# Kernel optimization log

Hardware: AMD Instinct MI355X
Metric: run time of the kernel (lower is better)

## Reference

```python
import jax, jax.numpy as jnp
import numpy as np

NUM_LEVEL = 16
LOG_T = 19
TABLE_SIZE = 2 ** LOG_T
FEAT = 2
MIN_RES = 16
MAX_RES = 512
N_POINTS = 262144

# [Teschner et al. 2003] spatial hash primes, wrapped to int32 like torch does
HASH_COEFFS = jnp.asarray(np.array([1, 2654435761, 805459861], dtype=np.uint32).astype(np.int32))


def _resolutions():
    coeff = (MAX_RES / MIN_RES) ** (1.0 / (NUM_LEVEL - 1))
    return jnp.floor(MIN_RES * (jnp.float32(coeff) ** jnp.arange(NUM_LEVEL, dtype=jnp.float32)))


def _spatial_hash(verts_i32):
    # verts_i32: (..., 3) int32; wrap-around int32 multiply then xor, then mod T (non-negative)
    x = HASH_COEFFS * verts_i32
    idx = jnp.bitwise_xor(jnp.bitwise_xor(x[..., 0], x[..., 1]), x[..., 2])
    return jnp.mod(idx, TABLE_SIZE)


def _hash_encode(coords, tables):
    # coords: (N,3) f32 in [0,1); tables: (L,T,F) f16
    res = _resolutions()                                   # (L,)
    scaled = coords[None, :, :] * res[:, None, None]        # (L,N,3)
    floor = jnp.floor(scaled)
    ceil = jnp.ceil(scaled)
    # 8 voxel corners via floor/ceil selection bits
    offs = jnp.asarray(np.array([[(o >> 2) & 1, (o >> 1) & 1, o & 1] for o in range(8)], dtype=np.bool_))
    sel = offs[:, None, None, :]                            # (8,1,1,3)
    corner = jnp.where(sel, ceil[None], floor[None])        # (8,L,N,3)
    comp = jnp.where(sel, floor[None], ceil[None])          # opposite corner (8,L,N,3)
    idx = _spatial_hash(corner.astype(jnp.int32))           # (8,L,N)
    # gather per-level features: tables[l][idx[:,l,:]] -> (L,8,N,F)
    feats = jax.vmap(lambda tab, i: tab[i], in_axes=(0, 1))(tables, idx)
    # trilinear weight of corner o = prod |opposite_corner - scaled|
    w = jnp.prod(jnp.abs(comp - scaled[None]), axis=-1)     # (8,L,N)
    w = jnp.transpose(w, (1, 0, 2))                         # (L,8,N)
    lvl = jnp.sum(feats.astype(jnp.float32) * w[..., None], axis=1)  # (L,N,F)
    return jnp.transpose(lvl, (1, 0, 2)).reshape(coords.shape[0], NUM_LEVEL * FEAT)


def _mlp(x, w_in, b_in, w_h0, b_h0, w_h1, b_h1, w_out, b_out):
    h = jax.nn.relu(x @ w_in.T + b_in)
    h = jax.nn.relu(h @ w_h0.T + b_h0)
    h = jax.nn.relu(h @ w_h1.T + b_h1)
    return h @ w_out.T + b_out


def setup_inputs() -> dict:
    key = jax.random.key(0)
    ks = jax.random.split(key, 8)
    coords = jax.random.uniform(ks[0], (N_POINTS, 3), dtype=jnp.float32)
    tables = (2e-4 * jax.random.uniform(ks[1], (NUM_LEVEL, TABLE_SIZE, FEAT), dtype=jnp.float32) - 1e-4).astype(jnp.float16)
    def lin(k, out_d, in_d):
        return jax.random.normal(k, (out_d, in_d), dtype=jnp.float32) * (1.0 / np.sqrt(in_d))
    return {
        'coords': coords, 'tables': tables,
        'w_in': lin(ks[2], 64, 32), 'b_in': jnp.zeros((64,), jnp.float32),
        'w_h0': lin(ks[3], 64, 64), 'b_h0': jnp.zeros((64,), jnp.float32),
        'w_h1': lin(ks[4], 64, 64), 'b_h1': jnp.zeros((64,), jnp.float32),
        'w_out': lin(ks[5], 16, 64), 'b_out': jnp.zeros((16,), jnp.float32),
    }


def reference(coords, tables, w_in, b_in, w_h0, b_h0, w_h1, b_h1, w_out, b_out):
    enc = _hash_encode(coords, tables)  # (N, 32)
    return _mlp(enc, w_in, b_in, w_h0, b_h0, w_h1, b_h1, w_out, b_out)  # (N, 16)
```

## Files before the change

kernel.cpp:

```cpp
#include <hip/hip_runtime.h>

#define NLVL 16
#define LOGT 19
#define TMASK ((1u << LOGT) - 1u)
#define SCALE 4096.0f
#define INV_SCALE (1.0f / 4096.0f)
#define NFRAG 22

typedef _Float16 half_t;
typedef half_t half8 __attribute__((ext_vector_type(8)));
typedef half_t half4 __attribute__((ext_vector_type(4)));
typedef half_t half2v __attribute__((ext_vector_type(2)));
typedef float  float4v __attribute__((ext_vector_type(4)));

__device__ __constant__ float RES_C[NLVL] = {16.f, 20.f, 25.f, 32.f, 40.f, 50.f, 64.f, 80.f,
                                             101.f, 128.f, 161.f, 203.f, 256.f, 322.f, 406.f, 512.f};

__device__ __forceinline__ float4v mfma16(half8 a, half8 b, float4v c) {
    return __builtin_amdgcn_mfma_f32_16x16x32_f16(a, b, c, 0, 0, 0);
}

__global__ __launch_bounds__(64, 1) void nerf_wprep(
    const float* __restrict__ w_in, const float* __restrict__ w_h0,
    const float* __restrict__ w_h1, const float* __restrict__ w_out,
    half8* __restrict__ frags)
{
    const int frag = blockIdx.x;
    const int lane = threadIdx.x;
    const int m    = lane & 15;
    const int quad = lane >> 4;

    const float* W; int ncol, row, col;
    if (frag < 4)       { W = w_in;  ncol = 32; row = frag * 16 + m;            col = quad * 8; }
    else if (frag < 12) { const int f = frag - 4;
                          W = w_h0;  ncol = 64; row = (f >> 1) * 16 + m;        col = (f & 1) * 32 + quad * 8; }
    else if (frag < 20) { const int f = frag - 12;
                          W = w_h1;  ncol = 64; row = (f >> 1) * 16 + m;        col = (f & 1) * 32 + quad * 8; }
    else                { const int f = frag - 20;
                          W = w_out; ncol = 64; row = m;                        col = f * 32 + quad * 8; }

    const float* p = W + row * ncol + col;
    half8 r;
    #pragma unroll
    for (int j = 0; j < 8; ++j) r[j] = (half_t)p[j];
    frags[frag * 64 + lane] = r;
}

__global__ __launch_bounds__(256, 8) void nerf_encode_pair2(
    const float* __restrict__ coords,
    const float2* __restrict__ tab,
    half_t* __restrict__ encT, int npts)
{
    const int bpl  = npts >> 8;
    const int l    = blockIdx.x / bpl;
    const int side = threadIdx.x & 1;
    const int base = (blockIdx.x % bpl) * 256 + (threadIdx.x >> 1);
    const int p0 = base, p1 = base + 128;

    const float r = RES_C[l];
    const float2* __restrict__ bp = tab + (((unsigned)l) << LOGT);

    const float ax = coords[p0 * 3 + 0] * r, ay = coords[p0 * 3 + 1] * r, az = coords[p0 * 3 + 2] * r;
    const float afx = floorf(ax), afy = floorf(ay), afz = floorf(az);
    const float agx = ceilf(ax),  agy = ceilf(ay),  agz = ceilf(az);
    const unsigned ahx = side ? (unsigned)(int)agx : (unsigned)(int)afx;
    const float    awx = side ? (ax - afx) : (agx - ax);
    const unsigned ahfy = (unsigned)(int)afy * 2654435761u;
    const unsigned ahgy = (unsigned)(int)agy * 2654435761u;
    const unsigned ahfz = (unsigned)(int)afz * 805459861u;
    const unsigned ahgz = (unsigned)(int)agz * 805459861u;
    const float aty = ay - afy, atz = az - afz, auy = agy - ay, auz = agz - az;

    const float bx = coords[p1 * 3 + 0] * r, by = coords[p1 * 3 + 1] * r, bz = coords[p1 * 3 + 2] * r;
    const float bfx = floorf(bx), bfy = floorf(by), bfz = floorf(bz);
    const float bgx = ceilf(bx),  bgy = ceilf(by),  bgz = ceilf(bz);
    const unsigned bhx = side ? (unsigned)(int)bgx : (unsigned)(int)bfx;
    const float    bwx = side ? (bx - bfx) : (bgx - bx);
    const unsigned bhfy = (unsigned)(int)bfy * 2654435761u;
    const unsigned bhgy = (unsigned)(int)bgy * 2654435761u;
    const unsigned bhfz = (unsigned)(int)bfz * 805459861u;
    const unsigned bhgz = (unsigned)(int)bgz * 805459861u;
    const float bty = by - bfy, btz = bz - bfz, buy = bgy - by, buz = bgz - bz;

    const float2 a0 = bp[(ahx ^ ahfy ^ ahfz) & TMASK];
    const float2 a1 = bp[(ahx ^ ahfy ^ ahgz) & TMASK];
    const float2 a2 = bp[(ahx ^ ahgy ^ ahfz) & TMASK];
    const float2 a3 = bp[(ahx ^ ahgy ^ ahgz) & TMASK];
    const float2 b0 = bp[(bhx ^ bhfy ^ bhfz) & TMASK];
    const float2 b1 = bp[(bhx ^ bhfy ^ bhgz) & TMASK];
    const float2 b2 = bp[(bhx ^ bhgy ^ bhfz) & TMASK];
    const float2 b3 = bp[(bhx ^ bhgy ^ bhgz) & TMASK];

    const float aw0 = awx * auy * auz, aw1 = awx * auy * atz;
    const float aw2 = awx * aty * auz, aw3 = awx * aty * atz;
    const float bw0 = bwx * buy * buz, bw1 = bwx * buy * btz;
    const float bw2 = bwx * bty * buz, bw3 = bwx * bty * btz;

    float ae0 = aw0 * a0.x + aw1 * a1.x + aw2 * a2.x + aw3 * a3.x;
    float ae1 = aw0 * a0.y + aw1 * a1.y + aw2 * a2.y + aw3 * a3.y;
    float be0 = bw0 * b0.x + bw1 * b1.x + bw2 * b2.x + bw3 * b3.x;
    float be1 = bw0 * b0.y + bw1 * b1.y + bw2 * b2.y + bw3 * b3.y;

    ae0 += __shfl_xor(ae0, 1, 64);
    ae1 += __shfl_xor(ae1, 1, 64);
    be0 += __shfl_xor(be0, 1, 64);
    be1 += __shfl_xor(be1, 1, 64);

    if (side == 0) {
        half2v h0; h0[0] = (half_t)(ae0 * SCALE); h0[1] = (half_t)(ae1 * SCALE);
        half2v h1; h1[0] = (half_t)(be0 * SCALE); h1[1] = (half_t)(be1 * SCALE);
        *reinterpret_cast<half2v*>(&encT[((size_t)l * npts + p0) * 2]) = h0;
        *reinterpret_cast<half2v*>(&encT[((size_t)l * npts + p1) * 2]) = h1;
    }
}

__global__ __launch_bounds__(256, 2) void nerf_mlp4(
    const half_t* __restrict__ encT,
    const half8* __restrict__ frags,
    const float* __restrict__ b_in, const float* __restrict__ b_h0,
    const float* __restrict__ b_h1, const float* __restrict__ b_out,
    float* __restrict__ out, int npts)
{
    __shared__ half_t actS[4][2][64 * 64];

    const int t    = threadIdx.x;
    const int lane = t & 63;
    const int wv   = t >> 6;
    const int m    = lane & 15;
    const int quad = lane >> 4;

    const size_t pbase = (size_t)blockIdx.x * 256 + (size_t)wv * 64;

    half8 be[4];
    #pragma unroll
    for (int T = 0; T < 4; ++T) {
        #pragma unroll
        for (int d = 0; d < 4; ++d) {
            const int L = quad * 4 + d;
            const half2v v = *reinterpret_cast<const half2v*>(
                &encT[((size_t)L * npts + pbase + T * 16 + m) * 2]);
            be[T][d * 2 + 0] = v[0];
            be[T][d * 2 + 1] = v[1];
        }
    }

    half8 aL1[4], aL2[8], aL3[8], aL4[2];
    #pragma unroll
    for (int f = 0; f < 4; ++f) aL1[f] = frags[(0 + f) * 64 + lane];
    #pragma unroll
    for (int f = 0; f < 8; ++f) aL2[f] = frags[(4 + f) * 64 + lane];
    #pragma unroll
    for (int f = 0; f < 8; ++f) aL3[f] = frags[(12 + f) * 64 + lane];
    #pragma unroll
    for (int f = 0; f < 2; ++f) aL4[f] = frags[(20 + f) * 64 + lane];

    float4v bL1[4], bL2[4], bL3[4], bL4;
    #pragma unroll
    for (int mt = 0; mt < 4; ++mt) {
        bL1[mt] = *reinterpret_cast<const float4v*>(b_in + mt * 16 + quad * 4);
        bL2[mt] = *reinterpret_cast<const float4v*>(b_h0 + mt * 16 + quad * 4);
        bL3[mt] = *reinterpret_cast<const float4v*>(b_h1 + mt * 16 + quad * 4);
    }
    bL4 = *reinterpret_cast<const float4v*>(b_out + quad * 4);

    half_t* const ping = &actS[wv][0][0];
    half_t* const pong = &actS[wv][1][0];
    const float4v zero = {0.f, 0.f, 0.f, 0.f};

    auto storeTile = [&](half_t* buf, int lp, int mt, float4v acc, float4v bias) {
        half4 h4;
        #pragma unroll
        for (int r = 0; r < 4; ++r)
            h4[r] = (half_t)fmaxf(fmaf(bias[r], SCALE, acc[r]), 0.f);
        const int c16  = mt * 2 + (quad >> 1);
        const int phys = c16 ^ (lp & 7);
        *reinterpret_cast<half4*>(&buf[lp * 64 + phys * 8 + (quad & 1) * 4]) = h4;
    };
    auto loadB = [&](const half_t* buf, int lp, int h) -> half8 {
        const int phys = (h * 4 + quad) ^ (lp & 7);
        return *reinterpret_cast<const half8*>(&buf[lp * 64 + phys * 8]);
    };

    #pragma unroll
    for (int T = 0; T < 4; ++T) {
        const int lp = T * 16 + m;
        #pragma unroll
        for (int mt = 0; mt < 4; ++mt) {
            float4v acc = mfma16(aL1[mt], be[T], zero);
            storeTile(ping, lp, mt, acc, bL1[mt]);
        }
    }
    #pragma unroll
    for (int T = 0; T < 4; ++T) {
        const int lp = T * 16 + m;
        const half8 p0 = loadB(ping, lp, 0);
        const half8 p1 = loadB(ping, lp, 1);
        #pragma unroll
        for (int mt = 0; mt < 4; ++mt) {
            float4v acc = mfma16(aL2[mt * 2 + 0], p0, zero);
            acc         = mfma16(aL2[mt * 2 + 1], p1, acc);
            storeTile(pong, lp, mt, acc, bL2[mt]);
        }
    }
    #pragma unroll
    for (int T = 0; T < 4; ++T) {
        const int lp = T * 16 + m;
        const half8 p0 = loadB(pong, lp, 0);
        const half8 p1 = loadB(pong, lp, 1);
        #pragma unroll
        for (int mt = 0; mt < 4; ++mt) {
            float4v acc = mfma16(aL3[mt * 2 + 0], p0, zero);
            acc         = mfma16(aL3[mt * 2 + 1], p1, acc);
            storeTile(ping, lp, mt, acc, bL3[mt]);
        }
    }
    #pragma unroll
    for (int T = 0; T < 4; ++T) {
        const int lp = T * 16 + m;
        const half8 p0 = loadB(ping, lp, 0);
        const half8 p1 = loadB(ping, lp, 1);
        float4v acc = mfma16(aL4[0], p0, zero);
        acc         = mfma16(aL4[1], p1, acc);
        float4v res;
        #pragma unroll
        for (int r = 0; r < 4; ++r)
            res[r] = fmaf(acc[r], INV_SCALE, bL4[r]);
        *reinterpret_cast<float4v*>(out + (pbase + lp) * 16 + quad * 4) = res;
    }
}

__global__ __launch_bounds__(256, 2) void nerf_fused(
    const float* __restrict__ coords,
    const float2* __restrict__ tab,
    const float* __restrict__ w_in, const float* __restrict__ b_in,
    const float* __restrict__ w_h0, const float* __restrict__ b_h0,
    const float* __restrict__ w_h1, const float* __restrict__ b_h1,
    const float* __restrict__ w_out, const float* __restrict__ b_out,
    float* __restrict__ out, int npts)
{
    __shared__ half_t encS[256 * 40];
    __shared__ half_t actS[4][2][32 * 64];

    const int t    = threadIdx.x;
    const int lane = t & 63;
    const int wv   = t >> 6;
    const int m    = lane & 15;
    const int quad = lane >> 4;
    const int pt = blockIdx.x * 256 + t;

    {
        const float cx = coords[pt * 3 + 0];
        const float cy = coords[pt * 3 + 1];
        const float cz = coords[pt * 3 + 2];
        float enc[32];
        #pragma unroll
        for (int l = 0; l < NLVL; ++l) {
            const float r = RES_C[l];
            const float sx = cx * r, sy = cy * r, sz = cz * r;
            const float fx = floorf(sx), fy = floorf(sy), fz = floorf(sz);
            const float gx = ceilf(sx),  gy = ceilf(sy),  gz = ceilf(sz);
            const unsigned hfx = (unsigned)(int)fx;
            const unsigned hgx = (unsigned)(int)gx;
            const unsigned hfy = (unsigned)(int)fy * 2654435761u;
            const unsigned hgy = (unsigned)(int)gy * 2654435761u;
            const unsigned hfz = (unsigned)(int)fz * 805459861u;
            const unsigned hgz = (unsigned)(int)gz * 805459861u;
            const float tx = sx - fx, ty = sy - fy, tz = sz - fz;
            const float ux = gx - sx, uy = gy - sy, uz = gz - sz;
            const unsigned lbase = ((unsigned)l) << LOGT;
            float e0 = 0.f, e1 = 0.f;
            #pragma unroll
            for (int o = 0; o < 8; ++o) {
                const unsigned h = ((o & 4) ? hgx : hfx)
                                 ^ ((o & 2) ? hgy : hfy)
                                 ^ ((o & 1) ? hgz : hfz);
                const unsigned idx = h & TMASK;
                const float w = (((o & 4) ? tx : ux)
                              *  ((o & 2) ? ty : uy))
                              *  ((o & 1) ? tz : uz);
                const float2 fv = tab[lbase + idx];
                e0 = fmaf(w, fv.x, e0);
                e1 = fmaf(w, fv.y, e1);
            }
            enc[2 * l + 0] = e0;
            enc[2 * l + 1] = e1;
        }
        #pragma unroll
        for (int c = 0; c < 4; ++c) {
            half8 h8;
            #pragma unroll
            for (int j = 0; j < 8; ++j) h8[j] = (half_t)(enc[c * 8 + j] * SCALE);
            *reinterpret_cast<half8*>(&encS[t * 40 + c * 8]) = h8;
        }
    }

    auto loadA = [&](const float* __restrict__ W, int ncol, int row, int col) -> half8 {
        const float* p = W + row * ncol + col;
        const float4v lo = *reinterpret_cast<const float4v*>(p);
        const float4v hi = *reinterpret_cast<const float4v*>(p + 4);
        half8 r;
        r[0] = (half_t)lo[0]; r[1] = (half_t)lo[1]; r[2] = (half_t)lo[2]; r[3] = (half_t)lo[3];
        r[4] = (half_t)hi[0]; r[5] = (half_t)hi[1]; r[6] = (half_t)hi[2]; r[7] = (half_t)hi[3];
        return r;
    };

    half8 aL1[4], aL2[8], aL3[8], aL4[2];
    #pragma unroll
    for (int mt = 0; mt < 4; ++mt) aL1[mt] = loadA(w_in, 32, mt * 16 + m, quad * 8);
    #pragma unroll
    for (int mt = 0; mt < 4; ++mt) {
        aL2[mt * 2 + 0] = loadA(w_h0, 64, mt * 16 + m, 0 * 32 + quad * 8);
        aL2[mt * 2 + 1] = loadA(w_h0, 64, mt * 16 + m, 1 * 32 + quad * 8);
        aL3[mt * 2 + 0] = loadA(w_h1, 64, mt * 16 + m, 0 * 32 + quad * 8);
        aL3[mt * 2 + 1] = loadA(w_h1, 64, mt * 16 + m, 1 * 32 + quad * 8);
    }
    aL4[0] = loadA(w_out, 64, m, 0 * 32 + quad * 8);
    aL4[1] = loadA(w_out, 64, m, 1 * 32 + quad * 8);

    float4v bL1[4], bL2[4], bL3[4], bL4;
    #pragma unroll
    for (int mt = 0; mt < 4; ++mt) {
        bL1[mt] = *reinterpret_cast<const float4v*>(b_in + mt * 16 + quad * 4);
        bL2[mt] = *reinterpret_cast<const float4v*>(b_h0 + mt * 16 + quad * 4);
        bL3[mt] = *reinterpret_cast<const float4v*>(b_h1 + mt * 16 + quad * 4);
    }
    bL4 = *reinterpret_cast<const float4v*>(b_out + quad * 4);

    half_t* const ping = &actS[wv][0][0];
    half_t* const pong = &actS[wv][1][0];
    const float4v zero = {0.f, 0.f, 0.f, 0.f};

    auto storeTile = [&](half_t* buf, int lp, int mt, float4v acc, float4v bias) {
        half4 h4;
        #pragma unroll
        for (int r = 0; r < 4; ++r)
            h4[r] = (half_t)fmaxf(fmaf(bias[r], SCALE, acc[r]), 0.f);
        const int c16  = mt * 2 + (quad >> 1);
        const int phys = c16 ^ (lp & 7);
        *reinterpret_cast<half4*>(&buf[lp * 64 + phys * 8 + (quad & 1) * 4]) = h4;
    };
    auto loadB = [&](const half_t* buf, int lp, int h) -> half8 {
        const int phys = (h * 4 + quad) ^ (lp & 7);
        return *reinterpret_cast<const half8*>(&buf[lp * 64 + phys * 8]);
    };

    for (int g = 0; g < 2; ++g) {
        #pragma unroll
        for (int nt = 0; nt < 2; ++nt) {
            const int lp   = nt * 16 + m;
            const int prow = wv * 64 + g * 32 + lp;
            const half8 bfr = *reinterpret_cast<const half8*>(&encS[prow * 40 + quad * 8]);
            #pragma unroll
            for (int mt = 0; mt < 4; ++mt) {
                float4v acc = mfma16(aL1[mt], bfr, zero);
                storeTile(ping, lp, mt, acc, bL1[mt]);
            }
            {
                const half8 p0 = loadB(ping, lp, 0);
                const half8 p1 = loadB(ping, lp, 1);
                #pragma unroll
                for (int mt = 0; mt < 4; ++mt) {
                    float4v acc = mfma16(aL2[mt * 2 + 0], p0, zero);
                    acc         = mfma16(aL2[mt * 2 + 1], p1, acc);
                    storeTile(pong, lp, mt, acc, bL2[mt]);
                }
            }
            {
                const half8 p0 = loadB(pong, lp, 0);
                const half8 p1 = loadB(pong, lp, 1);
                #pragma unroll
                for (int mt = 0; mt < 4; ++mt) {
                    float4v acc = mfma16(aL3[mt * 2 + 0], p0, zero);
                    acc         = mfma16(aL3[mt * 2 + 1], p1, acc);
                    storeTile(ping, lp, mt, acc, bL3[mt]);
                }
            }
            {
                const half8 p0 = loadB(ping, lp, 0);
                const half8 p1 = loadB(ping, lp, 1);
                float4v acc = mfma16(aL4[0], p0, zero);
                acc         = mfma16(aL4[1], p1, acc);
                float4v res;
                #pragma unroll
                for (int r = 0; r < 4; ++r)
                    res[r] = fmaf(acc[r], INV_SCALE, bL4[r]);
                const size_t ptg = (size_t)blockIdx.x * 256 + (size_t)wv * 64 + g * 32 + lp;
                *reinterpret_cast<float4v*>(out + ptg * 16 + quad * 4) = res;
            }
        }
    }
}

extern "C" void kernel_launch(void* const* d_in, const int* in_sizes, int n_in,
                              void* d_out, int out_size, void* d_ws, size_t ws_size,
                              hipStream_t stream) {
    const float*  coords = (const float*)d_in[0];
    const float2* tables = (const float2*)d_in[1];
    const float*  w_in   = (const float*)d_in[2];
    const float*  b_in   = (const float*)d_in[3];
    const float*  w_h0   = (const float*)d_in[4];
    const float*  b_h0   = (const float*)d_in[5];
    const float*  w_h1   = (const float*)d_in[6];
    const float*  b_h1   = (const float*)d_in[7];
    const float*  w_out  = (const float*)d_in[8];
    const float*  b_out  = (const float*)d_in[9];
    float* out = (float*)d_out;

    const int npts = in_sizes[0] / 3;
    const size_t encBytes  = (size_t)npts * 32 * sizeof(half_t);
    const size_t fragBytes = (size_t)NFRAG * 64 * sizeof(half8);

    if (ws_size >= encBytes + fragBytes && (npts & 255) == 0) {
        half_t* encT  = (half_t*)d_ws;
        half8*  frags = (half8*)((char*)d_ws + encBytes);
        nerf_wprep<<<NFRAG, 64, 0, stream>>>(w_in, w_h0, w_h1, w_out, frags);
        const int bpl = npts >> 8;
        nerf_encode_pair2<<<bpl * NLVL, 256, 0, stream>>>(coords, tables, encT, npts);
        nerf_mlp4<<<npts / 256, 256, 0, stream>>>(encT, frags,
                                                  b_in, b_h0, b_h1, b_out,
                                                  out, npts);
    } else {
        nerf_fused<<<npts / 256, 256, 0, stream>>>(coords, tables,
                                                   w_in, b_in, w_h0, b_h0,
                                                   w_h1, b_h1, w_out, b_out,
                                                   out, npts);
    }
}
```

Baseline: 209.0 us.

## Sort points by Morton bin before hash encoding to improve gather locality

Adds a histogram, scan and scatter pass that counting-sorts the points by a 32^3 Morton-order spatial bin. The encoder then reads the sorted coordinates, and the MLP writes each result back through the permutation. Encode blocks are interleaved so that several levels of the same point block run at the same time. The goal is better cache locality for the random hash-table gathers on the coarse levels. In exchange it adds four small kernels, atomics, a memset and extra traffic for the sorted copy and the permutation, and the MLP's final stores become scattered.

```diff
diff --git a/kernel.cpp b/kernel.cpp
--- a/kernel.cpp
+++ b/kernel.cpp
@@ -6,6 +6,7 @@
 #define SCALE 4096.0f
 #define INV_SCALE (1.0f / 4096.0f)
 #define NFRAG 22
+#define NBINS 32768
 
 typedef _Float16 half_t;
 typedef half_t half8 __attribute__((ext_vector_type(8)));
@@ -18,6 +19,20 @@
 
 __device__ __forceinline__ float4v mfma16(half8 a, half8 b, float4v c) {
     return __builtin_amdgcn_mfma_f32_16x16x32_f16(a, b, c, 0, 0, 0);
+}
+
+__device__ __forceinline__ unsigned spread5(unsigned x) {
+    x &= 31u;
+    x = (x | (x << 8)) & 0x100Fu;
+    x = (x | (x << 4)) & 0x10C3u;
+    x = (x | (x << 2)) & 0x1249u;
+    return x;
+}
+__device__ __forceinline__ unsigned bin3(float cx, float cy, float cz) {
+    const unsigned bx = min(31u, (unsigned)(cx * 32.f));
+    const unsigned by = min(31u, (unsigned)(cy * 32.f));
+    const unsigned bz = min(31u, (unsigned)(cz * 32.f));
+    return spread5(bx) | (spread5(by) << 1) | (spread5(bz) << 2);
 }
 
 __global__ __launch_bounds__(64, 1) void nerf_wprep(
@@ -46,21 +61,74 @@
     frags[frag * 64 + lane] = r;
 }
 
-__global__ __launch_bounds__(256, 8) void nerf_encode_pair2(
-    const float* __restrict__ coords,
+__global__ __launch_bounds__(256, 8) void nerf_hist(
+    const float* __restrict__ coords, unsigned* __restrict__ hist, int npts)
+{
+    const int p = blockIdx.x * 256 + threadIdx.x;
+    if (p >= npts) return;
+    const unsigned b = bin3(coords[p * 3 + 0], coords[p * 3 + 1], coords[p * 3 + 2]);
+    atomicAdd(&hist[b], 1u);
+}
+
+__global__ __launch_bounds__(256, 1) void nerf_scan(
+    const unsigned* __restrict__ hist, unsigned* __restrict__ offs)
+{
+    __shared__ unsigned part[256];
+    const int t = threadIdx.x;
+    unsigned s = 0;
+    for (int i = 0; i < NBINS / 256; ++i) s += hist[t * (NBINS / 256) + i];
+    part[t] = s;
+    __syncthreads();
+    for (int off = 1; off < 256; off <<= 1) {
+        const unsigned v = (t >= off) ? part[t - off] : 0u;
+        __syncthreads();
+        part[t] += v;
+        __syncthreads();
+    }
+    unsigned run = part[t] - s;
+    for (int i = 0; i < NBINS / 256; ++i) {
+        const unsigned c = hist[t * (NBINS / 256) + i];
+        offs[t * (NBINS / 256) + i] = run;
+        run += c;
+    }
+}
+
+__global__ __launch_bounds__(256, 8) void nerf_scatter(
+    const float* __restrict__ coords, unsigned* __restrict__ offs,
+    int* __restrict__ perm, float* __restrict__ sc, int npts)
+{
+    const int p = blockIdx.x * 256 + threadIdx.x;
+    if (p >= npts) return;
+    const float cx = coords[p * 3 + 0];
+    const float cy = coords[p * 3 + 1];
+    const float cz = coords[p * 3 + 2];
+    const unsigned b = bin3(cx, cy, cz);
+    const unsigned pos = atomicAdd(&offs[b], 1u);
+    perm[pos] = p;
+    sc[pos * 3 + 0] = cx;
+    sc[pos * 3 + 1] = cy;
+    sc[pos * 3 + 2] = cz;
+}
+
+__global__ __launch_bounds__(256, 8) void nerf_encode_sort(
+    const float* __restrict__ sc,
     const float2* __restrict__ tab,
     half_t* __restrict__ encT, int npts)
 {
-    const int bpl  = npts >> 8;
-    const int l    = blockIdx.x / bpl;
+    const int b     = blockIdx.x;
+    const int halfg = (int)(gridDim.x >> 1);
+    const int hi    = (b >= halfg) ? 1 : 0;
+    const int l     = (b & 7) + (hi << 3);
+    const int pb    = (hi ? (b - halfg) : b) >> 3;
+
     const int side = threadIdx.x & 1;
-    const int base = (blockIdx.x % bpl) * 256 + (threadIdx.x >> 1);
-    const int p0 = base, p1 = base + 128;
+    const int p0   = pb * 256 + ((threadIdx.x >> 1) << 1);
+    const int p1   = p0 + 1;
 
     const float r = RES_C[l];
     const float2* __restrict__ bp = tab + (((unsigned)l) << LOGT);
 
-    const float ax = coords[p0 * 3 + 0] * r, ay = coords[p0 * 3 + 1] * r, az = coords[p0 * 3 + 2] * r;
+    const float ax = sc[p0 * 3 + 0] * r, ay = sc[p0 * 3 + 1] * r, az = sc[p0 * 3 + 2] * r;
     const float afx = floorf(ax), afy = floorf(ay), afz = floorf(az);
     const float agx = ceilf(ax),  agy = ceilf(ay),  agz = ceilf(az);
     const unsigned ahx = side ? (unsigned)(int)agx : (unsigned)(int)afx;
@@ -71,7 +139,7 @@
     const unsigned ahgz = (unsigned)(int)agz * 805459861u;
     const float aty = ay - afy, atz = az - afz, auy = agy - ay, auz = agz - az;
 
-    const float bx = coords[p1 * 3 + 0] * r, by = coords[p1 * 3 + 1] * r, bz = coords[p1 * 3 + 2] * r;
+    const float bx = sc[p1 * 3 + 0] * r, by = sc[p1 * 3 + 1] * r, bz = sc[p1 * 3 + 2] * r;
     const float bfx = floorf(bx), bfy = floorf(by), bfz = floorf(bz);
     const float bgx = ceilf(bx),  bgy = ceilf(by),  bgz = ceilf(bz);
     const unsigned bhx = side ? (unsigned)(int)bgx : (unsigned)(int)bfx;
@@ -107,21 +175,22 @@
     be1 += __shfl_xor(be1, 1, 64);
 
     if (side == 0) {
-        half2v h0; h0[0] = (half_t)(ae0 * SCALE); h0[1] = (half_t)(ae1 * SCALE);
-        half2v h1; h1[0] = (half_t)(be0 * SCALE); h1[1] = (half_t)(be1 * SCALE);
-        *reinterpret_cast<half2v*>(&encT[((size_t)l * npts + p0) * 2]) = h0;
-        *reinterpret_cast<half2v*>(&encT[((size_t)l * npts + p1) * 2]) = h1;
+        half4 hv;
+        hv[0] = (half_t)(ae0 * SCALE); hv[1] = (half_t)(ae1 * SCALE);
+        hv[2] = (half_t)(be0 * SCALE); hv[3] = (half_t)(be1 * SCALE);
+        *reinterpret_cast<half4*>(&encT[((size_t)l * npts + p0) * 2]) = hv;
     }
 }
 
 __global__ __launch_bounds__(256, 2) void nerf_mlp4(
     const half_t* __restrict__ encT,
     const half8* __restrict__ frags,
+    const int* __restrict__ perm,
     const float* __restrict__ b_in, const float* __restrict__ b_h0,
     const float* __restrict__ b_h1, const float* __restrict__ b_out,
     float* __restrict__ out, int npts)
 {
-    __shared__ half_t actS[4][2][64 * 64];
+    __shared__ half_t actS[4][64 * 64];
 
     const int t    = threadIdx.x;
     const int lane = t & 63;
@@ -144,6 +213,10 @@
         }
     }
 
+    int pid[4];
+    #pragma unroll
+    for (int T = 0; T < 4; ++T) pid[T] = perm[pbase + T * 16 + m];
+
     half8 aL1[4], aL2[8], aL3[8], aL4[2];
     #pragma unroll
     for (int f = 0; f < 4; ++f) aL1[f] = frags[(0 + f) * 64 + lane];
@@ -163,11 +236,10 @@
     }
     bL4 = *reinterpret_cast<const float4v*>(b_out + quad * 4);
 
-    half_t* const ping = &actS[wv][0][0];
-    half_t* const pong = &actS[wv][1][0];
+    half_t* const buf = &actS[wv][0];
     const float4v zero = {0.f, 0.f, 0.f, 0.f};
 
-    auto storeTile = [&](half_t* buf, int lp, int mt, float4v acc, float4v bias) {
+    auto storeTile = [&](int lp, int mt, float4v acc, float4v bias) {
         half4 h4;
         #pragma unroll
         for (int r = 0; r < 4; ++r)
@@ -176,7 +248,7 @@
         const int phys = c16 ^ (lp & 7);
         *reinterpret_cast<half4*>(&buf[lp * 64 + phys * 8 + (quad & 1) * 4]) = h4;
     };
-    auto loadB = [&](const half_t* buf, int lp, int h) -> half8 {
+    auto loadB = [&](int lp, int h) -> half8 {
         const int phys = (h * 4 + quad) ^ (lp & 7);
         return *reinterpret_cast<const half8*>(&buf[lp * 64 + phys * 8]);
     };
@@ -187,45 +259,45 @@
         #pragma unroll
         for (int mt = 0; mt < 4; ++mt) {
             float4v acc = mfma16(aL1[mt], be[T], zero);
-            storeTile(ping, lp, mt, acc, bL1[mt]);
+            storeTile(lp, mt, acc, bL1[mt]);
         }
     }
     #pragma unroll
     for (int T = 0; T < 4; ++T) {
         const int lp = T * 16 + m;
-        const half8 p0 = loadB(ping, lp, 0);
-        const half8 p1 = loadB(ping, lp, 1);
+        const half8 p0 = loadB(lp, 0);
+        const half8 p1 = loadB(lp, 1);
         #pragma unroll
         for (int mt = 0; mt < 4; ++mt) {
             float4v acc = mfma16(aL2[mt * 2 + 0], p0, zero);
             acc         = mfma16(aL2[mt * 2 + 1], p1, acc);
-            storeTile(pong, lp, mt, acc, bL2[mt]);
+            storeTile(lp, mt, acc, bL2[mt]);
         }
     }
     #pragma unroll
     for (int T = 0; T < 4; ++T) {
         const int lp = T * 16 + m;
-        const half8 p0 = loadB(pong, lp, 0);
-        const half8 p1 = loadB(pong, lp, 1);
+        const half8 p0 = loadB(lp, 0);
+        const half8 p1 = loadB(lp, 1);
         #pragma unroll
         for (int mt = 0; mt < 4; ++mt) {
             float4v acc = mfma16(aL3[mt * 2 + 0], p0, zero);
             acc         = mfma16(aL3[mt * 2 + 1], p1, acc);
-            storeTile(ping, lp, mt, acc, bL3[mt]);
+            storeTile(lp, mt, acc, bL3[mt]);
         }
     }
     #pragma unroll
     for (int T = 0; T < 4; ++T) {
         const int lp = T * 16 + m;
-        const half8 p0 = loadB(ping, lp, 0);
-        const half8 p1 = loadB(ping, lp, 1);
+        const half8 p0 = loadB(lp, 0);
+        const half8 p1 = loadB(lp, 1);
         float4v acc = mfma16(aL4[0], p0, zero);
         acc         = mfma16(aL4[1], p1, acc);
         float4v res;
         #pragma unroll
         for (int r = 0; r < 4; ++r)
             res[r] = fmaf(acc[r], INV_SCALE, bL4[r]);
-        *reinterpret_cast<float4v*>(out + (pbase + lp) * 16 + quad * 4) = res;
+        *reinterpret_cast<float4v*>(out + (size_t)pid[T] * 16 + quad * 4) = res;
     }
 }
 
@@ -409,14 +481,28 @@
     const int npts = in_sizes[0] / 3;
     const size_t encBytes  = (size_t)npts * 32 * sizeof(half_t);
     const size_t fragBytes = (size_t)NFRAG * 64 * sizeof(half8);
-
-    if (ws_size >= encBytes + fragBytes && (npts & 255) == 0) {
-        half_t* encT  = (half_t*)d_ws;
-        half8*  frags = (half8*)((char*)d_ws + encBytes);
+    const size_t histBytes = (size_t)NBINS * 4;
+    const size_t offBytes  = (size_t)NBINS * 4;
+    const size_t permBytes = (size_t)npts * 4;
+    const size_t scBytes   = (size_t)npts * 12;
+    const size_t need = encBytes + fragBytes + histBytes + offBytes + permBytes + scBytes;
+
+    if (ws_size >= need && (npts & 255) == 0) {
+        char* w = (char*)d_ws;
+        half_t*   encT  = (half_t*)w;    w += encBytes;
+        half8*    frags = (half8*)w;     w += fragBytes;
+        unsigned* hist  = (unsigned*)w;  w += histBytes;
+        unsigned* offs  = (unsigned*)w;  w += offBytes;
+        int*      perm  = (int*)w;       w += permBytes;
+        float*    sc    = (float*)w;
+
+        hipMemsetAsync(hist, 0, histBytes, stream);
         nerf_wprep<<<NFRAG, 64, 0, stream>>>(w_in, w_h0, w_h1, w_out, frags);
-        const int bpl = npts >> 8;
-        nerf_encode_pair2<<<bpl * NLVL, 256, 0, stream>>>(coords, tables, encT, npts);
-        nerf_mlp4<<<npts / 256, 256, 0, stream>>>(encT, frags,
+        nerf_hist<<<npts / 256, 256, 0, stream>>>(coords, hist, npts);
+        nerf_scan<<<1, 256, 0, stream>>>(hist, offs);
+        nerf_scatter<<<npts / 256, 256, 0, stream>>>(coords, offs, perm, sc, npts);
+        nerf_encode_sort<<<(npts >> 8) * NLVL, 256, 0, stream>>>(sc, tables, encT, npts);
+        nerf_mlp4<<<npts / 256, 256, 0, stream>>>(encT, frags, perm,
                                                   b_in, b_h0, b_h1, b_out,
                                                   out, npts);
     } else {
```

Result: slower. 222.2 us (+6.3%).
